# Performance work log

Measured on AMD Instinct MI355X. Metric: run time of the kernel, lower is better.

The kernel has to match this reference:

```python
import jax, jax.numpy as jnp
import numpy as np

N_NODES = 50000
N_EDGES = 800000
IN_DIM, HID_DIM, OUT_DIM = 128, 256, 40


def setup_inputs() -> dict:
    key = jax.random.key(0)
    ks = jax.random.split(key, 8)
    x = jax.random.normal(ks[0], (N_NODES, IN_DIM), dtype=jnp.float32)
    edge_index = jax.random.randint(ks[1], (2, N_EDGES), 0, N_NODES, dtype=jnp.int64)
    s1 = 1.0 / np.sqrt(IN_DIM)
    s2 = 1.0 / np.sqrt(HID_DIM)
    return {
        "x": x,
        "edge_index": edge_index,
        "W1_l": jax.random.normal(ks[2], (IN_DIM, HID_DIM), dtype=jnp.float32) * s1,
        "W1_r": jax.random.normal(ks[3], (IN_DIM, HID_DIM), dtype=jnp.float32) * s1,
        "b1": jnp.zeros((HID_DIM,), dtype=jnp.float32),
        "W2_l": jax.random.normal(ks[4], (HID_DIM, OUT_DIM), dtype=jnp.float32) * s2,
        "W2_r": jax.random.normal(ks[5], (HID_DIM, OUT_DIM), dtype=jnp.float32) * s2,
        "b2": jnp.zeros((OUT_DIM,), dtype=jnp.float32),
    }


def _sage_conv(x, src, dst, W_l, W_r, b, n_nodes):
    # mean aggregation of source features onto destination nodes
    agg = jax.ops.segment_sum(x[src], dst, num_segments=n_nodes)  # [N, d]
    cnt = jax.ops.segment_sum(jnp.ones(src.shape[0], x.dtype), dst, num_segments=n_nodes)
    agg = agg / jnp.maximum(cnt, 1.0)[:, None]
    # PyG SAGEConv: lin_l(aggr) + lin_r(x), bias in lin_l
    return agg @ W_l + x @ W_r + b


def reference(x, edge_index, W1_l, W1_r, b1, W2_l, W2_r, b2):
    src, dst = edge_index[0], edge_index[1]
    n = x.shape[0]
    h = jax.nn.relu(_sage_conv(x, src, dst, W1_l, W1_r, b1, n))
    # dropout is identity in eval mode
    out = _sage_conv(h, src, dst, W2_l, W2_r, b2, n)
    return jax.nn.log_softmax(out, axis=1)
```

## Files before the change

### kernel.cpp

```cpp
#include <hip/hip_runtime.h>
#include <hip/hip_bf16.h>

#define N_NODES 50000
#define N_EDGES 800000
#define IN_DIM 128
#define HID_DIM 256
#define OUT_DIM 40
#define M_PAD 50048
#define NBUCKETS 782
#define EPB 8192
#define BINA_BLOCKS 98
#define BLK_PAD 128
#define CONVX_BLOCKS 3125

#define OFF_RP     0
#define OFF_ESRC   200064
#define OFF_STAGE  3400064
#define OFF_HISTG  6600064
#define OFF_PFXG   7000448
#define OFF_BTOT   7400832
#define OFF_BBASE  7403968
#define OFF_AB     7407104
#define OFF_W1T    33031680
#define OFF_W2T    33162752
#define OFF_P2     33203712
#define OFF_R2     37207552

typedef __attribute__((ext_vector_type(8))) short short8;
typedef __attribute__((ext_vector_type(4))) float f32x4;

__device__ __forceinline__ float bfu2f(unsigned u) {
  union { unsigned i; float f; } c; c.i = u << 16; return c.f;
}
__device__ __forceinline__ unsigned f2bfu(float f) {
  union { float f; unsigned i; } c; c.f = f;
  return (c.i + 0x7fffu + ((c.i >> 16) & 1u)) >> 16;
}

#define GLOAD_LDS16(g, l)                                                      \
  __builtin_amdgcn_global_load_lds(                                            \
      (const __attribute__((address_space(1))) void*)(g),                      \
      (__attribute__((address_space(3))) void*)(l), 16, 0, 0)

__global__ __launch_bounds__(1024) void k_hist(const int* __restrict__ dst,
                                               int* __restrict__ hist_g) {
  __shared__ int hist[NBUCKETS];
  int t = threadIdx.x, blk = blockIdx.x;
  for (int b = t; b < NBUCKETS; b += 1024) hist[b] = 0;
  __syncthreads();
  int e0 = blk * EPB, e1 = min(e0 + EPB, N_EDGES);
  for (int e = e0 + t; e < e1; e += 1024) atomicAdd(&hist[dst[e] >> 6], 1);
  __syncthreads();
  for (int b = t; b < NBUCKETS; b += 1024) hist_g[b * BLK_PAD + blk] = hist[b];
}

__global__ __launch_bounds__(256) void k_hscanA(const int* __restrict__ hist_g,
                                                int* __restrict__ pfx_g,
                                                int* __restrict__ btot) {
  int wave = blockIdx.x * 4 + (threadIdx.x >> 6);
  int lane = threadIdx.x & 63;
  if (wave >= NBUCKETS) return;
  const int* h = hist_g + wave * BLK_PAD;
  int v0 = (lane < BINA_BLOCKS) ? h[lane] : 0;
  int v1 = (lane + 64 < BINA_BLOCKS) ? h[lane + 64] : 0;
  int s0 = v0;
#pragma unroll
  for (int d = 1; d < 64; d <<= 1) {
    int u = __shfl_up(s0, d, 64);
    if (lane >= d) s0 += u;
  }
  int tot0 = __shfl(s0, 63, 64);
  int s1 = v1;
#pragma unroll
  for (int d = 1; d < 64; d <<= 1) {
    int u = __shfl_up(s1, d, 64);
    if (lane >= d) s1 += u;
  }
  s1 += tot0;
  pfx_g[wave * BLK_PAD + lane] = s0 - v0;
  if (lane + 64 < BLK_PAD) pfx_g[wave * BLK_PAD + lane + 64] = s1 - v1;
  if (lane == 63) btot[wave] = s1;
}

__global__ __launch_bounds__(1024) void k_hscanB(const int* __restrict__ btot,
                                                 int* __restrict__ bbase,
                                                 int* __restrict__ row_ptr) {
  __shared__ int part[1024];
  int t = threadIdx.x;
  int v = (t < NBUCKETS) ? btot[t] : 0;
  part[t] = v;
  __syncthreads();
  for (int off = 1; off < 1024; off <<= 1) {
    int u = (t >= off) ? part[t - off] : 0;
    __syncthreads();
    part[t] += u;
    __syncthreads();
  }
  if (t < NBUCKETS) bbase[t] = part[t] - v;
  if (t == NBUCKETS - 1) {
    bbase[NBUCKETS] = part[t];
    row_ptr[N_NODES] = part[t];
  }
}

__global__ __launch_bounds__(1024) void k_fill2(const int* __restrict__ src,
                                                const int* __restrict__ dst,
                                                const int* __restrict__ bbase,
                                                const int* __restrict__ pfx_g,
                                                unsigned* __restrict__ stage) {
  __shared__ int cur[NBUCKETS];
  int t = threadIdx.x, blk = blockIdx.x;
  for (int b = t; b < NBUCKETS; b += 1024)
    cur[b] = bbase[b] + pfx_g[b * BLK_PAD + blk];
  __syncthreads();
  int e0 = blk * EPB, e1 = min(e0 + EPB, N_EDGES);
  for (int e = e0 + t; e < e1; e += 1024) {
    int d = dst[e];
    int pos = atomicAdd(&cur[d >> 6], 1);
    stage[pos] = ((unsigned)src[e] << 6) | (unsigned)(d & 63);
  }
}

__global__ __launch_bounds__(256) void k_bsort(const unsigned* __restrict__ stage,
                                               const int* __restrict__ bbase,
                                               int* __restrict__ row_ptr,
                                               int* __restrict__ esrc) {
  __shared__ int lcnt[64];
  __shared__ int lout[1536];
  int b = blockIdx.x, t = threadIdx.x;
  int base = bbase[b];
  int nb = bbase[b + 1] - base;
  if (t < 64) lcnt[t] = 0;
  __syncthreads();
  const unsigned* sp = stage + base;
  for (int e = t; e < nb; e += 256) atomicAdd(&lcnt[sp[e] & 63u], 1);
  __syncthreads();
  if (t < 64) {
    int v = lcnt[t];
    int s = v;
#pragma unroll
    for (int d = 1; d < 64; d <<= 1) {
      int u = __shfl_up(s, d, 64);
      if (t >= d) s += u;
    }
    int node = b * 64 + t;
    if (node < N_NODES) row_ptr[node] = base + s - v;
    lcnt[t] = s - v;
  }
  __syncthreads();
  for (int e = t; e < nb; e += 256) {
    unsigned p = sp[e];
    int lp = atomicAdd(&lcnt[p & 63u], 1);
    lout[lp] = (int)(p >> 6);
  }
  __syncthreads();
  for (int i = t; i < nb; i += 256) esrc[base + i] = lout[i];
}

__global__ __launch_bounds__(256) void k_conv(const float* __restrict__ x,
                                              char* __restrict__ ABb,
                                              const float* __restrict__ W1l,
                                              const float* __restrict__ W1r,
                                              const float* __restrict__ W2l,
                                              const float* __restrict__ W2r,
                                              unsigned short* __restrict__ Wt1,
                                              unsigned short* __restrict__ Wt2) {
  if (blockIdx.x < CONVX_BLOCKS) {
    int t = blockIdx.x * 256 + threadIdx.x;
    int row = t >> 4, c8 = (t & 15) << 3;
    const float* xp = x + (size_t)row * IN_DIM + c8;
    unsigned short o[8];
#pragma unroll
    for (int i = 0; i < 8; ++i) o[i] = (unsigned short)f2bfu(xp[i]);
    *(short8*)(ABb + (size_t)row * 512 + 256 + c8 * 2) = *(short8*)o;
  } else if (blockIdx.x < CONVX_BLOCKS + 256) {
    int n = blockIdx.x - CONVX_BLOCKS;
    int k = threadIdx.x;
    float v = (k < 128) ? W1l[(size_t)k * HID_DIM + n]
                        : W1r[(size_t)(k - 128) * HID_DIM + n];
    Wt1[(size_t)n * 256 + k] = (unsigned short)f2bfu(v);
  } else {
    int n = blockIdx.x - CONVX_BLOCKS - 256;
    int k = threadIdx.x;
    float v = (n < OUT_DIM) ? W2l[(size_t)k * OUT_DIM + n]
                            : W2r[(size_t)k * OUT_DIM + (n - OUT_DIM)];
    Wt2[(size_t)n * 256 + k] = (unsigned short)f2bfu(v);
  }
}

__global__ __launch_bounds__(256) void k_agg1(char* __restrict__ ABb,
    const int* __restrict__ row_ptr, const int* __restrict__ esrc) {
  int tid = threadIdx.x;
  int node = blockIdx.x * 4 + (tid >> 6);
  int lane = tid & 63;
  int g = lane >> 4;
  int q = lane & 15;
  int beg = row_ptr[node], end = row_ptr[node + 1];
  float s[8];
#pragma unroll
  for (int j = 0; j < 8; ++j) s[j] = 0.f;

  for (int e0 = beg; e0 < end; e0 += 8) {
    int eA = e0 + g;
    int eB = eA + 4;
    int iA = min(eA, end - 1);
    int iB = min(eB, end - 1);
    int sA = esrc[iA], sB = esrc[iB];
    float wA = (eA < end) ? 1.f : 0.f;
    float wB = (eB < end) ? 1.f : 0.f;
    short8 vA = *(const short8*)(ABb + (size_t)sA * 512 + 256 + q * 16);
    short8 vB = *(const short8*)(ABb + (size_t)sB * 512 + 256 + q * 16);
#pragma unroll
    for (int j = 0; j < 8; ++j)
      s[j] = fmaf(wA, bfu2f((unsigned short)vA[j]), s[j]);
#pragma unroll
    for (int j = 0; j < 8; ++j)
      s[j] = fmaf(wB, bfu2f((unsigned short)vB[j]), s[j]);
  }
#pragma unroll
  for (int j = 0; j < 8; ++j) {
    s[j] += __shfl_xor(s[j], 16, 64);
    s[j] += __shfl_xor(s[j], 32, 64);
  }
  float inv = 1.0f / (float)max(end - beg, 1);
  if (lane < 16) {
    unsigned short o[8];
#pragma unroll
    for (int j = 0; j < 8; ++j) o[j] = (unsigned short)f2bfu(s[j] * inv);
    *(short8*)(ABb + (size_t)node * 512 + q * 16) = *(short8*)o;
  }
}

__global__ __launch_bounds__(256) void k_gemm(
    const char* __restrict__ ABb, const short* __restrict__ Wt1,
    const short* __restrict__ Wt2, const float* __restrict__ b1,
    const float* __restrict__ b2, unsigned short* __restrict__ P2,
    float* __restrict__ R2) {
  __shared__ __align__(16) char As[64 * 512];
  const int tid = threadIdx.x;
  const int w = tid >> 6, lane = tid & 63;
  const int row0 = blockIdx.x * 64;

  {
    const char* gbase = ABb + (size_t)row0 * 512;
#pragma unroll
    for (int i = 0; i < 8; ++i) {
      int o = i * 4096 + w * 1024 + lane * 16;
      int row = o >> 9;
      int kslot = ((o & 511) >> 4) ^ (row & 7);
      GLOAD_LDS16(gbase + row * 512 + kslot * 16, As + i * 4096 + w * 1024);
    }
  }
  __syncthreads();

  f32x4 acc[4][4];
#pragma unroll
  for (int mi = 0; mi < 4; ++mi)
#pragma unroll
    for (int ni = 0; ni < 4; ++ni) acc[mi][ni] = (f32x4){0.f, 0.f, 0.f, 0.f};

  const short* wb1 = Wt1 + (size_t)(w * 64 + (lane & 15)) * 256 + (lane >> 4) * 8;

  for (int ks = 0; ks < 8; ++ks) {
    short8 af[4], bf[4];
#pragma unroll
    for (int mi = 0; mi < 4; ++mi) {
      int row = mi * 16 + (lane & 15);
      int kslot = (ks * 4 + (lane >> 4)) ^ (row & 7);
      af[mi] = *(const short8*)(As + row * 512 + kslot * 16);
    }
#pragma unroll
    for (int ni = 0; ni < 4; ++ni)
      bf[ni] = *(const short8*)(wb1 + ni * 16 * 256 + ks * 32);
#pragma unroll
    for (int mi = 0; mi < 4; ++mi)
#pragma unroll
      for (int ni = 0; ni < 4; ++ni)
        acc[mi][ni] = __builtin_amdgcn_mfma_f32_16x16x32_bf16(
            af[mi], bf[ni], acc[mi][ni], 0, 0, 0);
  }

  __syncthreads();

#pragma unroll
  for (int ni = 0; ni < 4; ++ni) {
    int col = w * 64 + ni * 16 + (lane & 15);
    float bv = b1[col];
#pragma unroll
    for (int mi = 0; mi < 4; ++mi) {
#pragma unroll
      for (int r = 0; r < 4; ++r) {
        int row = mi * 16 + (lane >> 4) * 4 + r;
        float v = fmaxf(acc[mi][ni][r] + bv, 0.f);
        int gr = (col >> 3) ^ (row & 7);
        *(unsigned short*)(As + row * 512 + gr * 16 + (col & 7) * 2) =
            (unsigned short)f2bfu(v);
      }
    }
  }
  __syncthreads();

  f32x4 acc2[5];
#pragma unroll
  for (int ni = 0; ni < 5; ++ni) acc2[ni] = (f32x4){0.f, 0.f, 0.f, 0.f};

  const short* wb2 = Wt2 + (size_t)(lane & 15) * 256 + (lane >> 4) * 8;
  const int arow = w * 16 + (lane & 15);

  for (int ks = 0; ks < 8; ++ks) {
    int kslot = (ks * 4 + (lane >> 4)) ^ (arow & 7);
    short8 a = *(const short8*)(As + arow * 512 + kslot * 16);
#pragma unroll
    for (int ni = 0; ni < 5; ++ni) {
      short8 bf = *(const short8*)(wb2 + ni * 16 * 256 + ks * 32);
      acc2[ni] = __builtin_amdgcn_mfma_f32_16x16x32_bf16(a, bf, acc2[ni], 0, 0, 0);
    }
  }

#pragma unroll
  for (int ni = 0; ni < 5; ++ni) {
    int col = ni * 16 + (lane & 15);
#pragma unroll
    for (int r = 0; r < 4; ++r) {
      int row = row0 + w * 16 + (lane >> 4) * 4 + r;
      float v = acc2[ni][r];
      if (col < OUT_DIM) {
        P2[(size_t)row * OUT_DIM + col] = (unsigned short)f2bfu(v);
      } else {
        R2[(size_t)row * OUT_DIM + (col - OUT_DIM)] = v + b2[col - OUT_DIM];
      }
    }
  }
}

__global__ __launch_bounds__(256) void k_agg2(const unsigned short* __restrict__ P2,
    const float* __restrict__ R2, const int* __restrict__ row_ptr,
    const int* __restrict__ esrc, float* __restrict__ out) {
  int tid = threadIdx.x;
  int node = blockIdx.x * 4 + (tid >> 6);
  int lane = tid & 63;
  int g = lane >> 3;
  int q = lane & 7;
  int beg = row_ptr[node], end = row_ptr[node + 1];
  float s[8];
#pragma unroll
  for (int j = 0; j < 8; ++j) s[j] = 0.f;

  for (int e0 = beg; e0 < end; e0 += 8) {
    int e = e0 + g;
    if (e < end && q < 5) {
      int srcn = esrc[e];
      short8 v = *(const short8*)((const char*)P2 + (size_t)srcn * 80 + q * 16);
#pragma unroll
      for (int j = 0; j < 8; ++j)
        s[j] += bfu2f((unsigned short)v[j]);
    }
  }
#pragma unroll
  for (int j = 0; j < 8; ++j) {
    s[j] += __shfl_xor(s[j], 8, 64);
    s[j] += __shfl_xor(s[j], 16, 64);
    s[j] += __shfl_xor(s[j], 32, 64);
  }

  float inv = 1.0f / (float)max(end - beg, 1);
  float v[8];
  float m = -1e30f;
  if (q < 5) {
    const float* rr = R2 + (size_t)node * OUT_DIM + q * 8;
    f32x4 r0 = *(const f32x4*)rr;
    f32x4 r1 = *(const f32x4*)(rr + 4);
#pragma unroll
    for (int j = 0; j < 8; ++j) {
      float rj = (j < 4) ? r0[j] : r1[j - 4];
      v[j] = s[j] * inv + rj;
      m = fmaxf(m, v[j]);
    }
  }
#pragma unroll
  for (int o = 1; o <= 4; o <<= 1) m = fmaxf(m, __shfl_xor(m, o, 64));
  float ex = 0.f;
  if (q < 5) {
#pragma unroll
    for (int j = 0; j < 8; ++j) ex += __expf(v[j] - m);
  }
#pragma unroll
  for (int o = 1; o <= 4; o <<= 1) ex += __shfl_xor(ex, o, 64);
  float ls = __logf(ex) + m;

  if (g == 0 && q < 5) {
    float* op = out + (size_t)node * OUT_DIM + q * 8;
    f32x4 o0, o1;
#pragma unroll
    for (int j = 0; j < 4; ++j) { o0[j] = v[j] - ls; o1[j] = v[j + 4] - ls; }
    *(f32x4*)op = o0;
    *(f32x4*)(op + 4) = o1;
  }
}

extern "C" void kernel_launch(void* const* d_in, const int* in_sizes, int n_in,
                              void* d_out, int out_size, void* d_ws, size_t ws_size,
                              hipStream_t stream) {
  const float* x   = (const float*)d_in[0];
  const int*   ei  = (const int*)d_in[1];
  const float* W1l = (const float*)d_in[2];
  const float* W1r = (const float*)d_in[3];
  const float* b1  = (const float*)d_in[4];
  const float* W2l = (const float*)d_in[5];
  const float* W2r = (const float*)d_in[6];
  const float* b2  = (const float*)d_in[7];
  float* out = (float*)d_out;

  const int* src = ei;
  const int* dst = ei + N_EDGES;

  char* ws = (char*)d_ws;
  int*      row_ptr = (int*)(ws + OFF_RP);
  int*      esrc    = (int*)(ws + OFF_ESRC);
  unsigned* stage   = (unsigned*)(ws + OFF_STAGE);
  int*      hist_g  = (int*)(ws + OFF_HISTG);
  int*      pfx_g   = (int*)(ws + OFF_PFXG);
  int*      btot    = (int*)(ws + OFF_BTOT);
  int*      bbase   = (int*)(ws + OFF_BBASE);
  char*     ABb     = ws + OFF_AB;
  unsigned short* Wt1 = (unsigned short*)(ws + OFF_W1T);
  unsigned short* Wt2 = (unsigned short*)(ws + OFF_W2T);
  unsigned short* P2  = (unsigned short*)(ws + OFF_P2);
  float* R2 = (float*)(ws + OFF_R2);

  (void)hipMemsetAsync(ABb + (size_t)N_NODES * 512, 0, (M_PAD - N_NODES) * 512,
                       stream);

  k_conv<<<CONVX_BLOCKS + 336, 256, 0, stream>>>(x, ABb, W1l, W1r, W2l, W2r,
                                                 Wt1, Wt2);

  k_hist<<<BINA_BLOCKS, 1024, 0, stream>>>(dst, hist_g);
  k_hscanA<<<(NBUCKETS + 3) / 4, 256, 0, stream>>>(hist_g, pfx_g, btot);
  k_hscanB<<<1, 1024, 0, stream>>>(btot, bbase, row_ptr);
  k_fill2<<<BINA_BLOCKS, 1024, 0, stream>>>(src, dst, bbase, pfx_g, stage);
  k_bsort<<<NBUCKETS, 256, 0, stream>>>(stage, bbase, row_ptr, esrc);

  k_agg1<<<N_NODES / 4, 256, 0, stream>>>(ABb, row_ptr, esrc);
  k_gemm<<<M_PAD / 64, 256, 0, stream>>>(ABb, (const short*)Wt1,
                                         (const short*)Wt2, b1, b2, P2, R2);
  k_agg2<<<N_NODES / 4, 256, 0, stream>>>(P2, R2, row_ptr, esrc, out);
}
```

Baseline: 212.0 us.

## Widen fused GEMM to 512 threads, stage outputs through LDS, fold pad memset

The fused two-layer GEMM kernel now runs with 8 waves per block instead of 4. Each wave computes half as many layer-1 output columns, which cuts accumulator registers, and the second-layer tiles are split across wave pairs. Layer-2 results are staged in shared memory and written back as coalesced 16-byte stores, replacing the scattered 2- and 4-byte global writes. The separate memset that zeroed the padding rows is replaced by an extra block in the conversion kernel, saving one launch. The cost is an extra barrier and uneven work across waves in the second GEMM.

```diff
diff --git a/kernel.cpp b/kernel.cpp
--- a/kernel.cpp
+++ b/kernel.cpp
@@ -179,12 +179,18 @@
     float v = (k < 128) ? W1l[(size_t)k * HID_DIM + n]
                         : W1r[(size_t)(k - 128) * HID_DIM + n];
     Wt1[(size_t)n * 256 + k] = (unsigned short)f2bfu(v);
-  } else {
+  } else if (blockIdx.x < CONVX_BLOCKS + 336) {
     int n = blockIdx.x - CONVX_BLOCKS - 256;
     int k = threadIdx.x;
     float v = (n < OUT_DIM) ? W2l[(size_t)k * OUT_DIM + n]
                             : W2r[(size_t)k * OUT_DIM + (n - OUT_DIM)];
     Wt2[(size_t)n * 256 + k] = (unsigned short)f2bfu(v);
+  } else {
+    char* pad = ABb + (size_t)N_NODES * 512;
+    f32x4 z = (f32x4){0.f, 0.f, 0.f, 0.f};
+#pragma unroll
+    for (int i = 0; i < 6; ++i)
+      *(f32x4*)(pad + (threadIdx.x * 6 + i) * 16) = z;
   }
 }
 
@@ -231,7 +237,7 @@
   }
 }
 
-__global__ __launch_bounds__(256) void k_gemm(
+__global__ __launch_bounds__(512) void k_gemm(
     const char* __restrict__ ABb, const short* __restrict__ Wt1,
     const short* __restrict__ Wt2, const float* __restrict__ b1,
     const float* __restrict__ b2, unsigned short* __restrict__ P2,
@@ -244,25 +250,25 @@
   {
     const char* gbase = ABb + (size_t)row0 * 512;
 #pragma unroll
-    for (int i = 0; i < 8; ++i) {
-      int o = i * 4096 + w * 1024 + lane * 16;
+    for (int i = 0; i < 4; ++i) {
+      int o = i * 8192 + w * 1024 + lane * 16;
       int row = o >> 9;
       int kslot = ((o & 511) >> 4) ^ (row & 7);
-      GLOAD_LDS16(gbase + row * 512 + kslot * 16, As + i * 4096 + w * 1024);
-    }
-  }
-  __syncthreads();
-
-  f32x4 acc[4][4];
+      GLOAD_LDS16(gbase + row * 512 + kslot * 16, As + i * 8192 + w * 1024);
+    }
+  }
+  __syncthreads();
+
+  f32x4 acc[4][2];
 #pragma unroll
   for (int mi = 0; mi < 4; ++mi)
 #pragma unroll
-    for (int ni = 0; ni < 4; ++ni) acc[mi][ni] = (f32x4){0.f, 0.f, 0.f, 0.f};
-
-  const short* wb1 = Wt1 + (size_t)(w * 64 + (lane & 15)) * 256 + (lane >> 4) * 8;
+    for (int ni = 0; ni < 2; ++ni) acc[mi][ni] = (f32x4){0.f, 0.f, 0.f, 0.f};
+
+  const short* wb1 = Wt1 + (size_t)(w * 32 + (lane & 15)) * 256 + (lane >> 4) * 8;
 
   for (int ks = 0; ks < 8; ++ks) {
-    short8 af[4], bf[4];
+    short8 af[4], bf[2];
 #pragma unroll
     for (int mi = 0; mi < 4; ++mi) {
       int row = mi * 16 + (lane & 15);
@@ -270,12 +276,12 @@
       af[mi] = *(const short8*)(As + row * 512 + kslot * 16);
     }
 #pragma unroll
-    for (int ni = 0; ni < 4; ++ni)
+    for (int ni = 0; ni < 2; ++ni)
       bf[ni] = *(const short8*)(wb1 + ni * 16 * 256 + ks * 32);
 #pragma unroll
     for (int mi = 0; mi < 4; ++mi)
 #pragma unroll
-      for (int ni = 0; ni < 4; ++ni)
+      for (int ni = 0; ni < 2; ++ni)
         acc[mi][ni] = __builtin_amdgcn_mfma_f32_16x16x32_bf16(
             af[mi], bf[ni], acc[mi][ni], 0, 0, 0);
   }
@@ -283,8 +289,8 @@
   __syncthreads();
 
 #pragma unroll
-  for (int ni = 0; ni < 4; ++ni) {
-    int col = w * 64 + ni * 16 + (lane & 15);
+  for (int ni = 0; ni < 2; ++ni) {
+    int col = w * 32 + ni * 16 + (lane & 15);
     float bv = b1[col];
 #pragma unroll
     for (int mi = 0; mi < 4; ++mi) {
@@ -300,36 +306,53 @@
   }
   __syncthreads();
 
-  f32x4 acc2[5];
-#pragma unroll
-  for (int ni = 0; ni < 5; ++ni) acc2[ni] = (f32x4){0.f, 0.f, 0.f, 0.f};
+  const int rt = w >> 1;
+  const int ni0 = (w & 1) ? 3 : 0;
+  const int nin = (w & 1) ? 2 : 3;
+  f32x4 acc2[3];
+#pragma unroll
+  for (int i = 0; i < 3; ++i) acc2[i] = (f32x4){0.f, 0.f, 0.f, 0.f};
 
   const short* wb2 = Wt2 + (size_t)(lane & 15) * 256 + (lane >> 4) * 8;
-  const int arow = w * 16 + (lane & 15);
+  const int arow = rt * 16 + (lane & 15);
 
   for (int ks = 0; ks < 8; ++ks) {
     int kslot = (ks * 4 + (lane >> 4)) ^ (arow & 7);
     short8 a = *(const short8*)(As + arow * 512 + kslot * 16);
-#pragma unroll
-    for (int ni = 0; ni < 5; ++ni) {
-      short8 bf = *(const short8*)(wb2 + ni * 16 * 256 + ks * 32);
-      acc2[ni] = __builtin_amdgcn_mfma_f32_16x16x32_bf16(a, bf, acc2[ni], 0, 0, 0);
-    }
-  }
-
-#pragma unroll
-  for (int ni = 0; ni < 5; ++ni) {
-    int col = ni * 16 + (lane & 15);
-#pragma unroll
-    for (int r = 0; r < 4; ++r) {
-      int row = row0 + w * 16 + (lane >> 4) * 4 + r;
-      float v = acc2[ni][r];
-      if (col < OUT_DIM) {
-        P2[(size_t)row * OUT_DIM + col] = (unsigned short)f2bfu(v);
-      } else {
-        R2[(size_t)row * OUT_DIM + (col - OUT_DIM)] = v + b2[col - OUT_DIM];
+    for (int i = 0; i < 3; ++i) {
+      if (i < nin) {
+        short8 bf = *(const short8*)(wb2 + (ni0 + i) * 16 * 256 + ks * 32);
+        acc2[i] = __builtin_amdgcn_mfma_f32_16x16x32_bf16(a, bf, acc2[i], 0, 0, 0);
       }
     }
+  }
+
+  __syncthreads();
+
+  for (int i = 0; i < 3; ++i) {
+    if (i < nin) {
+      int col = (ni0 + i) * 16 + (lane & 15);
+#pragma unroll
+      for (int r = 0; r < 4; ++r) {
+        int row = rt * 16 + (lane >> 4) * 4 + r;
+        float v = acc2[i][r];
+        if (col < OUT_DIM) {
+          *(unsigned short*)(As + row * 80 + col * 2) = (unsigned short)f2bfu(v);
+        } else {
+          *(float*)(As + 5120 + row * 160 + (col - OUT_DIM) * 4) =
+              v + b2[col - OUT_DIM];
+        }
+      }
+    }
+  }
+  __syncthreads();
+
+  {
+    char* p2g = (char*)P2 + (size_t)row0 * 80;
+    if (tid < 320) *(f32x4*)(p2g + tid * 16) = *(const f32x4*)(As + tid * 16);
+    char* r2g = (char*)R2 + (size_t)row0 * 160;
+    for (int i = tid; i < 640; i += 512)
+      *(f32x4*)(r2g + i * 16) = *(const f32x4*)(As + 5120 + i * 16);
   }
 }
 
@@ -428,10 +451,7 @@
   unsigned short* P2  = (unsigned short*)(ws + OFF_P2);
   float* R2 = (float*)(ws + OFF_R2);
 
-  (void)hipMemsetAsync(ABb + (size_t)N_NODES * 512, 0, (M_PAD - N_NODES) * 512,
-                       stream);
-
-  k_conv<<<CONVX_BLOCKS + 336, 256, 0, stream>>>(x, ABb, W1l, W1r, W2l, W2r,
+  k_conv<<<CONVX_BLOCKS + 337, 256, 0, stream>>>(x, ABb, W1l, W1r, W2l, W2r,
                                                  Wt1, Wt2);
 
   k_hist<<<BINA_BLOCKS, 1024, 0, stream>>>(dst, hist_g);
@@ -441,7 +461,7 @@
   k_bsort<<<NBUCKETS, 256, 0, stream>>>(stage, bbase, row_ptr, esrc);
 
   k_agg1<<<N_NODES / 4, 256, 0, stream>>>(ABb, row_ptr, esrc);
-  k_gemm<<<M_PAD / 64, 256, 0, stream>>>(ABb, (const short*)Wt1,
+  k_gemm<<<M_PAD / 64, 512, 0, stream>>>(ABb, (const short*)Wt1,
                                          (const short*)Wt2, b1, b2, P2, R2);
   k_agg2<<<N_NODES / 4, 256, 0, stream>>>(P2, R2, row_ptr, esrc, out);
 }
```

Measured after the change: 209.6 us. About the same (-1.1%).
